# Optimization experiments

Measured on AMD Instinct MI355X. Metric: run time of the kernel, lower is better.

Reference implementation:

```python
import jax, jax.numpy as jnp
import numpy as np

N_HEAD = 16
N_KV_HEAD = 4
HEAD_DIM = 128  # n_embd // n_head = 2048 // 16


def _apply_rope(x, pos, T):
    # x: [B, H, T, D]; RoPE cache built exactly like the torch module:
    # cos/sin use repeat_interleave(2) on freqs, rotation uses half-split.
    D = x.shape[-1]
    half = D // 2
    inv_freq = 1.0 / jnp.power(10000.0, jnp.arange(0, D, 2, dtype=jnp.float32) / D)  # [half]
    t = jnp.arange(pos, pos + T, dtype=jnp.float32)                                  # [T]
    freqs = t[:, None] * inv_freq[None, :]                                           # [T, half]
    freqs = jnp.repeat(freqs, 2, axis=-1)                                            # [T, D]
    cos = jnp.cos(freqs)[None, None, :, :]
    sin = jnp.sin(freqs)[None, None, :, :]
    x1, x2 = x[..., :half], x[..., half:]
    rotated = jnp.concatenate([-x2, x1], axis=-1)
    return x * cos + rotated * sin


def setup_inputs() -> dict:
    key = jax.random.key(0)
    ks = jax.random.split(key, 5)
    B, T, E = 2, 2048, 2048
    KV = N_KV_HEAD * HEAD_DIM  # 512
    s = 0.02
    return {
        "x": jax.random.normal(ks[0], (B, T, E), dtype=jnp.float32),
        "Wq": jax.random.normal(ks[1], (E, E), dtype=jnp.float32) * s,
        "Wk": jax.random.normal(ks[2], (E, KV), dtype=jnp.float32) * s,
        "Wv": jax.random.normal(ks[3], (E, KV), dtype=jnp.float32) * s,
        "Wproj": jax.random.normal(ks[4], (E, E), dtype=jnp.float32) * s,
        "pos": 0,
    }


def reference(x, Wq, Wk, Wv, Wproj, pos):
    B, T, E = x.shape
    H, HKV, D = N_HEAD, N_KV_HEAD, HEAD_DIM
    G = H // HKV  # query heads per kv head

    q = (x @ Wq).reshape(B, T, H, D).transpose(0, 2, 1, 3)     # [B,H,T,D]
    k = (x @ Wk).reshape(B, T, HKV, D).transpose(0, 2, 1, 3)   # [B,HKV,T,D]
    v = (x @ Wv).reshape(B, T, HKV, D).transpose(0, 2, 1, 3)   # [B,HKV,T,D]

    q = _apply_rope(q, pos, T)
    k = _apply_rope(k, pos, T)

    # GQA: group query heads over shared kv heads
    qg = q.reshape(B, HKV, G, T, D)
    scale = 1.0 / jnp.sqrt(jnp.asarray(D, dtype=x.dtype))
    scores = jnp.einsum('bkgtd,bksd->bkgts', qg, k) * scale    # [B,HKV,G,T,T]

    causal = jnp.tril(jnp.ones((T, T), dtype=bool))
    scores = jnp.where(causal, scores, jnp.finfo(scores.dtype).min)
    attn = jax.nn.softmax(scores, axis=-1)

    out = jnp.einsum('bkgts,bksd->bkgtd', attn, v)             # [B,HKV,G,T,D]
    y = out.reshape(B, H, T, D).transpose(0, 2, 1, 3).reshape(B, T, E)
    return y @ Wproj
```

## Files before the change

### kernel.cpp

```cpp
#include <hip/hip_runtime.h>
#include <hip/hip_bf16.h>
#include <stdint.h>

typedef unsigned short u16;
typedef float f32x4 __attribute__((ext_vector_type(4)));
typedef __bf16 bf16x8 __attribute__((ext_vector_type(8)));
typedef unsigned short u16x8 __attribute__((ext_vector_type(8)));
typedef float f32x4v __attribute__((ext_vector_type(4)));

#define T_SEQ 2048

__device__ __forceinline__ u16 f2bf(float f) {
    unsigned int u = __float_as_uint(f);
    unsigned int r = (u + 0x7fffu + ((u >> 16) & 1u)) >> 16;
    return (u16)r;
}
__device__ __forceinline__ float bf2f(u16 b) {
    return __uint_as_float(((unsigned int)b) << 16);
}

__device__ __forceinline__ void gload_lds16(const void* g, void* l) {
    __builtin_amdgcn_global_load_lds(
        (__attribute__((address_space(1))) void*)(g),
        (__attribute__((address_space(3))) void*)(l), 16, 0, 0);
}

__global__ void cast_f32_bf16(const float* __restrict__ in, u16* __restrict__ out, int n8) {
    int i = blockIdx.x * blockDim.x + threadIdx.x;
    if (i >= n8) return;
    const f32x4v* p = (const f32x4v*)(in + (size_t)i * 8);
    f32x4v a = p[0], b = p[1];
    u16x8 v;
    v[0]=f2bf(a.x); v[1]=f2bf(a.y); v[2]=f2bf(a.z); v[3]=f2bf(a.w);
    v[4]=f2bf(b.x); v[5]=f2bf(b.y); v[6]=f2bf(b.z); v[7]=f2bf(b.w);
    *(u16x8*)(out + (size_t)i * 8) = v;
}

__global__ void transpose_cast(const float* __restrict__ W, u16* __restrict__ Wt, int N) {
    __shared__ alignas(16) float sW[64 * 68];
    const int t = threadIdx.x;
    const int k0 = blockIdx.x * 64, n0 = blockIdx.y * 64;
#pragma unroll
    for (int i = 0; i < 4; i++) {
        int kr = i * 16 + (t >> 4), nc = (t & 15) * 4;
        *(f32x4v*)&sW[kr * 68 + nc] = *(const f32x4v*)&W[(size_t)(k0 + kr) * N + n0 + nc];
    }
    __syncthreads();
#pragma unroll
    for (int i = 0; i < 2; i++) {
        int nr = i * 32 + (t >> 3), kc = (t & 7) * 8;
        u16x8 v;
#pragma unroll
        for (int j = 0; j < 8; j++) v[j] = f2bf(sW[(kc + j) * 68 + nr]);
        *(u16x8*)&Wt[(size_t)(n0 + nr) * 2048 + k0 + kc] = v;
    }
}

__device__ __forceinline__ void stage_rows(const u16* g, u16* lds, int R, int kcol0, int K, int t) {
    int row = R + (t >> 3);
    int u = t & 7;
    gload_lds16(g + (size_t)row * K + kcol0 + ((u ^ (row & 7)) * 8), lds + row * 64 + u * 8);
}
__device__ __forceinline__ void stage_half256(const u16* g, u16* lds, int half, int j, int kcol0, int K, int t) {
    int idx = j * 512 + t;
    int group = idx >> 8;
    int r32 = (idx >> 3) & 31;
    int row = group * 64 + half * 32 + r32;
    int u = idx & 7;
    gload_lds16(g + (size_t)row * K + kcol0 + ((u ^ (row & 7)) * 8), lds + row * 64 + u * 8);
}
__device__ __forceinline__ bf16x8 lds_ld(const u16* lds, int row, int kc, int hl) {
    return *(const bf16x8*)&lds[row * 64 + (((kc * 4 + hl) ^ (row & 7)) * 8)];
}

__global__ __launch_bounds__(512, 2) void gemm_qkv(const u16* __restrict__ A, const u16* __restrict__ Bt,
                                                   u16* __restrict__ C, int M, int N, int K) {
    __shared__ alignas(16) u16 ldsA[2][256 * 64];
    __shared__ alignas(16) u16 ldsB[2][192 * 64];
    const int t = threadIdx.x, wave = t >> 6, lane = t & 63;
    const int l15 = lane & 15, hl = lane >> 4;
    const int wr = wave >> 2, wc = wave & 3;

    const int f = blockIdx.x;
    const int swz = (f & 7) * 32 + (f >> 3);
    const int bx = swz & 15, by = swz >> 4;
    const int m0 = bx * 256, n0 = by * 192;

    const u16* gA = A + (size_t)m0 * K;
    const u16* gB = Bt + (size_t)n0 * K;

    f32x4 acc[8][3];
    f32x4 z = {0.f, 0.f, 0.f, 0.f};
#pragma unroll
    for (int m = 0; m < 8; m++)
#pragma unroll
        for (int n = 0; n < 3; n++) acc[m][n] = z;

    stage_rows(gA, ldsA[0], 0, 0, K, t);
    stage_rows(gA, ldsA[0], 128, 0, K, t);
    stage_rows(gB, ldsB[0], 0, 0, K, t);
    stage_rows(gB, ldsB[0], 64, 0, K, t);
    stage_rows(gB, ldsB[0], 128, 0, K, t);
    stage_rows(gA, ldsA[0], 64, 0, K, t);
    stage_rows(gA, ldsA[0], 192, 0, K, t);

    const int KT = K >> 6;
    for (int kt = 0; kt < KT; ++kt) {
        const int c = kt & 1;
        const int kn = (kt + 1 < KT) ? (kt + 1) * 64 : kt * 64;
        const u16* lAc = ldsA[c];
        const u16* lBc = ldsB[c];
        u16* lAn = ldsA[c ^ 1];
        u16* lBn = ldsB[c ^ 1];

        bf16x8 aF[4][2], bF[3][2];

        asm volatile("s_waitcnt vmcnt(2)" ::: "memory");
        __builtin_amdgcn_s_barrier();
#pragma unroll
        for (int mi = 0; mi < 4; mi++)
#pragma unroll
            for (int kc = 0; kc < 2; kc++)
                aF[mi][kc] = lds_ld(lAc, wr * 128 + mi * 16 + l15, kc, hl);
#pragma unroll
        for (int n = 0; n < 3; n++)
#pragma unroll
            for (int kc = 0; kc < 2; kc++)
                bF[n][kc] = lds_ld(lBc, wc * 48 + n * 16 + l15, kc, hl);
        stage_rows(gA, lAn, 0, kn, K, t);
        stage_rows(gA, lAn, 128, kn, K, t);
        stage_rows(gB, lBn, 0, kn, K, t);
        __builtin_amdgcn_s_setprio(1);
#pragma unroll
        for (int mi = 0; mi < 4; mi++)
#pragma unroll
            for (int n = 0; n < 3; n++)
#pragma unroll
                for (int kc = 0; kc < 2; kc++)
                    acc[mi][n] = __builtin_amdgcn_mfma_f32_16x16x32_bf16(aF[mi][kc], bF[n][kc], acc[mi][n], 0, 0, 0);
        __builtin_amdgcn_s_setprio(0);

        asm volatile("s_waitcnt vmcnt(3)" ::: "memory");
        __builtin_amdgcn_s_barrier();
#pragma unroll
        for (int mi = 0; mi < 4; mi++)
#pragma unroll
            for (int kc = 0; kc < 2; kc++)
                aF[mi][kc] = lds_ld(lAc, wr * 128 + 64 + mi * 16 + l15, kc, hl);
        stage_rows(gB, lBn, 64, kn, K, t);
        stage_rows(gB, lBn, 128, kn, K, t);
        stage_rows(gA, lAn, 64, kn, K, t);
        stage_rows(gA, lAn, 192, kn, K, t);
        __builtin_amdgcn_s_setprio(1);
#pragma unroll
        for (int mi = 0; mi < 4; mi++)
#pragma unroll
            for (int n = 0; n < 3; n++)
#pragma unroll
                for (int kc = 0; kc < 2; kc++)
                    acc[4 + mi][n] = __builtin_amdgcn_mfma_f32_16x16x32_bf16(aF[mi][kc], bF[n][kc], acc[4 + mi][n], 0, 0, 0);
        __builtin_amdgcn_s_setprio(0);
    }

#pragma unroll
    for (int m = 0; m < 8; m++)
#pragma unroll
        for (int n = 0; n < 3; n++)
#pragma unroll
            for (int r = 0; r < 4; r++) {
                int row = m0 + wr * 128 + m * 16 + hl * 4 + r;
                int col = n0 + wc * 48 + n * 16 + l15;
                C[(size_t)row * N + col] = f2bf(acc[m][n][r]);
            }
}

__global__ __launch_bounds__(512, 2) void gemm_proj(const u16* __restrict__ A, const u16* __restrict__ Bt,
                                                    float* __restrict__ C, int M, int N, int K) {
    __shared__ alignas(16) u16 ldsA[2][128 * 64];
    __shared__ alignas(16) u16 ldsB[2][256 * 64];
    const int t = threadIdx.x, wave = t >> 6, lane = t & 63;
    const int l15 = lane & 15, hl = lane >> 4;
    const int wr = wave >> 2, wc = wave & 3;

    const int f = blockIdx.x;
    const int swz = (f & 7) * 32 + (f >> 3);
    const int bx = swz & 31, by = swz >> 5;
    const int m0 = bx * 128, n0 = by * 256;

    const u16* gA = A + (size_t)m0 * K;
    const u16* gB = Bt + (size_t)n0 * K;

    f32x4 acc[4][4];
    f32x4 z = {0.f, 0.f, 0.f, 0.f};
#pragma unroll
    for (int m = 0; m < 4; m++)
#pragma unroll
        for (int n = 0; n < 4; n++) acc[m][n] = z;

    stage_rows(gA, ldsA[0], 0, 0, K, t);
    stage_rows(gA, ldsA[0], 64, 0, K, t);
    stage_half256(gB, ldsB[0], 0, 0, 0, K, t);
    stage_half256(gB, ldsB[0], 0, 1, 0, K, t);
    stage_half256(gB, ldsB[0], 1, 0, 0, K, t);
    stage_half256(gB, ldsB[0], 1, 1, 0, K, t);

    const int KT = K >> 6;
    for (int kt = 0; kt < KT; ++kt) {
        const int c = kt & 1;
        const int kn = (kt + 1 < KT) ? (kt + 1) * 64 : kt * 64;
        const u16* lAc = ldsA[c];
        const u16* lBc = ldsB[c];
        u16* lAn = ldsA[c ^ 1];
        u16* lBn = ldsB[c ^ 1];

        bf16x8 aF[4][2], bF[2][2];

        asm volatile("s_waitcnt vmcnt(2)" ::: "memory");
        __builtin_amdgcn_s_barrier();
#pragma unroll
        for (int mi = 0; mi < 4; mi++)
#pragma unroll
            for (int kc = 0; kc < 2; kc++)
                aF[mi][kc] = lds_ld(lAc, wr * 64 + mi * 16 + l15, kc, hl);
#pragma unroll
        for (int n = 0; n < 2; n++)
#pragma unroll
            for (int kc = 0; kc < 2; kc++)
                bF[n][kc] = lds_ld(lBc, wc * 64 + n * 16 + l15, kc, hl);
        stage_rows(gA, lAn, 0, kn, K, t);
        stage_rows(gA, lAn, 64, kn, K, t);
        stage_half256(gB, lBn, 0, 0, kn, K, t);
        stage_half256(gB, lBn, 0, 1, kn, K, t);
        __builtin_amdgcn_s_setprio(1);
#pragma unroll
        for (int mi = 0; mi < 4; mi++)
#pragma unroll
            for (int n = 0; n < 2; n++)
#pragma unroll
                for (int kc = 0; kc < 2; kc++)
                    acc[mi][n] = __builtin_amdgcn_mfma_f32_16x16x32_bf16(aF[mi][kc], bF[n][kc], acc[mi][n], 0, 0, 0);
        __builtin_amdgcn_s_setprio(0);

        asm volatile("s_waitcnt vmcnt(4)" ::: "memory");
        __builtin_amdgcn_s_barrier();
#pragma unroll
        for (int n = 0; n < 2; n++)
#pragma unroll
            for (int kc = 0; kc < 2; kc++)
                bF[n][kc] = lds_ld(lBc, wc * 64 + 32 + n * 16 + l15, kc, hl);
        stage_half256(gB, lBn, 1, 0, kn, K, t);
        stage_half256(gB, lBn, 1, 1, kn, K, t);
        __builtin_amdgcn_s_setprio(1);
#pragma unroll
        for (int mi = 0; mi < 4; mi++)
#pragma unroll
            for (int n = 0; n < 2; n++)
#pragma unroll
                for (int kc = 0; kc < 2; kc++)
                    acc[mi][2 + n] = __builtin_amdgcn_mfma_f32_16x16x32_bf16(aF[mi][kc], bF[n][kc], acc[mi][2 + n], 0, 0, 0);
        __builtin_amdgcn_s_setprio(0);
    }

#pragma unroll
    for (int m = 0; m < 4; m++)
#pragma unroll
        for (int n = 0; n < 4; n++)
#pragma unroll
            for (int r = 0; r < 4; r++) {
                int row = m0 + wr * 64 + m * 16 + hl * 4 + r;
                int col = n0 + wc * 64 + n * 16 + l15;
                C[(size_t)row * N + col] = acc[m][n][r];
            }
}

__global__ void rope_kernel(u16* __restrict__ qkv, const int* __restrict__ pos) {
    int tid = blockIdx.x * 256 + threadIdx.x;
    int j = tid & 63;
    int rest = tid >> 6;
    int slice = rest % 20;
    int row = rest / 20;
    if (row >= 2 * T_SEQ) return;
    float tpos = (float)((row % T_SEQ) + pos[0]);
    int base = (slice < 16) ? slice * 128 : 2048 + (slice - 16) * 128;
    u16* p = qkv + (size_t)row * 3072 + base;
    float x1 = bf2f(p[j]), x2 = bf2f(p[j + 64]);
    const float c0 = 0.20762050593045702f;
    int i = j >> 1;
    float fA = tpos * exp2f(-(float)i * c0);
    float fB = tpos * exp2f(-(float)(32 + i) * c0);
    float o1 = x1 * cosf(fA) - x2 * sinf(fA);
    float o2 = x2 * cosf(fB) + x1 * sinf(fB);
    p[j] = f2bf(o1);
    p[j + 64] = f2bf(o2);
}

__global__ void vtrans(const u16* __restrict__ qkv, u16* __restrict__ vt) {
    __shared__ alignas(16) u16 sT[64 * 72];
    const int t = threadIdx.x;
    const int t0 = blockIdx.x * 64;
    const int d0 = blockIdx.y * 64;
    const int kh = blockIdx.z & 3, b = blockIdx.z >> 2;
#pragma unroll
    for (int i = 0; i < 2; i++) {
        int tr = i * 32 + (t >> 3), dc = (t & 7) * 8;
        *(u16x8*)&sT[tr * 72 + dc] =
            *(const u16x8*)&qkv[(size_t)(b * T_SEQ + t0 + tr) * 3072 + 2560 + kh * 128 + d0 + dc];
    }
    __syncthreads();
#pragma unroll
    for (int i = 0; i < 2; i++) {
        int dr = i * 32 + (t >> 3), tc = (t & 7) * 8;
        u16x8 v;
#pragma unroll
        for (int j = 0; j < 8; j++) v[j] = sT[(tc + j) * 72 + dr];
        *(u16x8*)&vt[((size_t)(b * 4 + kh) * 128 + d0 + dr) * 2048 + t0 + tc] = v;
    }
}

__global__ __launch_bounds__(256, 2) void attn(const u16* __restrict__ qkv,
                                               const u16* __restrict__ vt,
                                               u16* __restrict__ out) {
    __shared__ alignas(16) u16 sK[2][8192];
    __shared__ alignas(16) u16 sV[8192];
    __shared__ alignas(16) u16 sP[4 * 32 * 72];
    const int t = threadIdx.x, wave = t >> 6, lane = t & 63;
    const int l15 = lane & 15, hl = lane >> 4;

    const int f = blockIdx.x;
    const int sel = f >> 8, u = f & 255;
    const int bkh = u & 7, b = bkh >> 2, kh = bkh & 3;
    const int h = kh * 4 + ((u >> 3) & 3);
    const int j = u >> 5;
    const int a = sel ? (15 - j) : j;
    const int q0 = a * 128;
    const int nt = 2 * a + 2;

    const float sc = 0.08838834764831845f;

    bf16x8 qf[2][4];
#pragma unroll
    for (int m = 0; m < 2; m++)
#pragma unroll
        for (int c = 0; c < 4; c++) {
            const u16* qp = qkv + (size_t)(b * T_SEQ + q0 + wave * 32 + m * 16 + l15) * 3072
                            + h * 128 + c * 32 + hl * 8;
            u16x8 raw = *(const u16x8*)qp;
            u16x8 sv_;
#pragma unroll
            for (int e = 0; e < 8; e++) sv_[e] = f2bf(bf2f(raw[e]) * sc);
            qf[m][c] = *(bf16x8*)&sv_;
        }

    u16x8 onesu;
#pragma unroll
    for (int e = 0; e < 8; e++) onesu[e] = 0x3F80;
    const bf16x8 onesf = *(bf16x8*)&onesu;

    float mrow[2][4];
    f32x4 o[2][8];
    f32x4 osum[2];
    f32x4 z = {0.f, 0.f, 0.f, 0.f};
#pragma unroll
    for (int m = 0; m < 2; m++) {
#pragma unroll
        for (int r = 0; r < 4; r++) mrow[m][r] = -1e30f;
        osum[m] = z;
#pragma unroll
        for (int n8 = 0; n8 < 8; n8++) o[m][n8] = z;
    }

    asm volatile("s_waitcnt vmcnt(0)" ::: "memory");

    const u16* kgbase = qkv + (size_t)(b * T_SEQ) * 3072 + 2048 + kh * 128;
    const u16* vgbase = vt + (size_t)(b * 4 + kh) * 128 * 2048;

#pragma unroll
    for (int p = 0; p < 4; p++) {
        int i = p * 256 + t;
        int row = i >> 4, c = i & 15;
        gload_lds16(kgbase + (size_t)row * 3072 + ((c ^ (row & 7)) * 8), (u16*)sK[0] + i * 8);
    }

    int cur = 0;
    for (int it = 0; it < nt; ++it) {
        const int kv0 = it * 64;
        const int kvn = (it + 1 < nt) ? kv0 + 64 : kv0;
#pragma unroll
        for (int p = 0; p < 4; p++) {
            int i = p * 256 + t;
            int row = i >> 3, c = i & 7;
            gload_lds16(vgbase + (size_t)row * 2048 + kv0 + ((c ^ (row & 7)) * 8), sV + i * 8);
        }
#pragma unroll
        for (int p = 0; p < 4; p++) {
            int i = p * 256 + t;
            int row = i >> 4, c = i & 15;
            gload_lds16(kgbase + (size_t)(kvn + row) * 3072 + ((c ^ (row & 7)) * 8),
                        (u16*)sK[cur ^ 1] + i * 8);
        }
        asm volatile("s_waitcnt vmcnt(8)" ::: "memory");
        __builtin_amdgcn_s_barrier();

        f32x4 sA[2][4];
#pragma unroll
        for (int m = 0; m < 2; m++)
#pragma unroll
            for (int n = 0; n < 4; n++) sA[m][n] = z;
#pragma unroll
        for (int n = 0; n < 4; n++)
#pragma unroll
            for (int c = 0; c < 4; c++) {
                int row = n * 16 + l15;
                bf16x8 kf = *(const bf16x8*)&sK[cur][row * 128 + (((c * 4 + hl) ^ (row & 7)) * 8)];
#pragma unroll
                for (int m = 0; m < 2; m++)
                    sA[m][n] = __builtin_amdgcn_mfma_f32_16x16x32_bf16(qf[m][c], kf, sA[m][n], 0, 0, 0);
            }

#pragma unroll
        for (int m = 0; m < 2; m++)
#pragma unroll
            for (int r = 0; r < 4; r++) {
                const int grow = q0 + wave * 32 + m * 16 + hl * 4 + r;
                float mv[4];
#pragma unroll
                for (int n = 0; n < 4; n++)
                    mv[n] = (kv0 + n * 16 + l15 <= grow) ? sA[m][n][r] : -1e30f;
                float pmax = fmaxf(fmaxf(mv[0], mv[1]), fmaxf(mv[2], mv[3]));
                if (__builtin_expect(__any(pmax > mrow[m][r] + 8.f), 0)) {
                    float mx = pmax;
#pragma unroll
                    for (int off = 1; off < 16; off <<= 1) mx = fmaxf(mx, __shfl_xor(mx, off));
                    float mnew = fmaxf(mrow[m][r], mx);
                    float alpha = __expf(mrow[m][r] - mnew);
                    mrow[m][r] = mnew;
#pragma unroll
                    for (int n8 = 0; n8 < 8; n8++) o[m][n8][r] *= alpha;
                    osum[m][r] *= alpha;
                }
#pragma unroll
                for (int n = 0; n < 4; n++)
                    sP[(wave * 32 + m * 16 + hl * 4 + r) * 72 + n * 16 + l15] =
                        f2bf(__expf(mv[n] - mrow[m][r]));
            }

        asm volatile("s_waitcnt vmcnt(4)" ::: "memory");
        __builtin_amdgcn_s_barrier();

        bf16x8 pa[2][2];
#pragma unroll
        for (int m = 0; m < 2; m++)
#pragma unroll
            for (int k2 = 0; k2 < 2; k2++)
                pa[m][k2] = *(const bf16x8*)&sP[(wave * 32 + m * 16 + l15) * 72 + k2 * 32 + hl * 8];
#pragma unroll
        for (int m = 0; m < 2; m++)
#pragma unroll
            for (int k2 = 0; k2 < 2; k2++)
                osum[m] = __builtin_amdgcn_mfma_f32_16x16x32_bf16(pa[m][k2], onesf, osum[m], 0, 0, 0);
#pragma unroll
        for (int n8 = 0; n8 < 8; n8++)
#pragma unroll
            for (int k2 = 0; k2 < 2; k2++) {
                int d = n8 * 16 + l15;
                bf16x8 vf = *(const bf16x8*)&sV[d * 64 + (((k2 * 4 + hl) ^ (d & 7)) * 8)];
#pragma unroll
                for (int m = 0; m < 2; m++)
                    o[m][n8] = __builtin_amdgcn_mfma_f32_16x16x32_bf16(pa[m][k2], vf, o[m][n8], 0, 0, 0);
            }
        __builtin_amdgcn_s_barrier();
        cur ^= 1;
    }

#pragma unroll
    for (int m = 0; m < 2; m++)
#pragma unroll
        for (int r = 0; r < 4; r++) {
            float inv = 1.f / osum[m][r];
            int orow = b * T_SEQ + q0 + wave * 32 + m * 16 + hl * 4 + r;
#pragma unroll
            for (int n8 = 0; n8 < 8; n8++)
                out[(size_t)orow * 2048 + h * 128 + n8 * 16 + l15] = f2bf(o[m][n8][r] * inv);
        }
}

extern "C" void kernel_launch(void* const* d_in, const int* in_sizes, int n_in,
                              void* d_out, int out_size, void* d_ws, size_t ws_size,
                              hipStream_t stream) {
    const float* x  = (const float*)d_in[0];
    const float* Wq = (const float*)d_in[1];
    const float* Wk = (const float*)d_in[2];
    const float* Wv = (const float*)d_in[3];
    const float* Wp = (const float*)d_in[4];
    const int*   pos = (const int*)d_in[5];

    char* ws = (char*)d_ws;
    u16* xbf   = (u16*)(ws);
    u16* WtQKV = (u16*)(ws + 16777216);
    u16* WtP   = (u16*)(ws + 29360128);
    u16* QKV   = (u16*)(ws + 37748736);
    u16* Vt    = (u16*)(ws + 62914560);
    u16* AO    = (u16*)(ws + 67108864);

    cast_f32_bf16<<<4096, 256, 0, stream>>>(x, xbf, 1048576);
    transpose_cast<<<dim3(32, 32), 256, 0, stream>>>(Wq, WtQKV, 2048);
    transpose_cast<<<dim3(32, 8), 256, 0, stream>>>(Wk, WtQKV + (size_t)2048 * 2048, 512);
    transpose_cast<<<dim3(32, 8), 256, 0, stream>>>(Wv, WtQKV + (size_t)2560 * 2048, 512);
    transpose_cast<<<dim3(32, 32), 256, 0, stream>>>(Wp, WtP, 2048);

    gemm_qkv<<<256, 512, 0, stream>>>(xbf, WtQKV, QKV, 4096, 3072, 2048);
    rope_kernel<<<20480, 256, 0, stream>>>(QKV, pos);
    vtrans<<<dim3(32, 2, 8), 256, 0, stream>>>(QKV, Vt);
    attn<<<512, 256, 0, stream>>>(QKV, Vt, AO);
    gemm_proj<<<256, 512, 0, stream>>>(AO, WtP, (float*)d_out, 4096, 2048, 2048);
}
```

Before: 212.1 us.

## Load V fragments directly into registers and drop V shared-memory staging

The attention kernel now reads V^T fragments straight from global memory into 16 registers per lane each iteration, instead of staging them through a swizzled LDS buffer. This frees the V LDS buffer and removes two of the three barriers per iteration. It also switches the bf16 conversions to hardware casts. The cost is higher register pressure under the launch_bounds(256,2) limit and uncoalesced global loads that each wave repeats. The barrier removal relies on sP being wave-private, and on the sK double buffer staying race-free with a single barrier per iteration.

New measurement: 257.3 us. 1.21x slower.

```diff
diff --git a/kernel.cpp b/kernel.cpp
--- a/kernel.cpp
+++ b/kernel.cpp
@@ -17,6 +17,10 @@
 }
 __device__ __forceinline__ float bf2f(u16 b) {
     return __uint_as_float(((unsigned int)b) << 16);
+}
+__device__ __forceinline__ u16 bfbits(float f) {
+    __bf16 h = (__bf16)f;
+    return __builtin_bit_cast(u16, h);
 }
 
 __device__ __forceinline__ void gload_lds16(const void* g, void* l) {
@@ -321,8 +325,7 @@
                                                const u16* __restrict__ vt,
                                                u16* __restrict__ out) {
     __shared__ alignas(16) u16 sK[2][8192];
-    __shared__ alignas(16) u16 sV[8192];
-    __shared__ alignas(16) u16 sP[4 * 32 * 72];
+    __shared__ alignas(16) __bf16 sP[4 * 32 * 72];
     const int t = threadIdx.x, wave = t >> 6, lane = t & 63;
     const int l15 = lane & 15, hl = lane >> 4;
 
@@ -372,7 +375,7 @@
     asm volatile("s_waitcnt vmcnt(0)" ::: "memory");
 
     const u16* kgbase = qkv + (size_t)(b * T_SEQ) * 3072 + 2048 + kh * 128;
-    const u16* vgbase = vt + (size_t)(b * 4 + kh) * 128 * 2048;
+    const u16* vbase = vt + ((size_t)(b * 4 + kh) * 128 + l15) * 2048 + hl * 8;
 
 #pragma unroll
     for (int p = 0; p < 4; p++) {
@@ -385,12 +388,17 @@
     for (int it = 0; it < nt; ++it) {
         const int kv0 = it * 64;
         const int kvn = (it + 1 < nt) ? kv0 + 64 : kv0;
-#pragma unroll
-        for (int p = 0; p < 4; p++) {
-            int i = p * 256 + t;
-            int row = i >> 3, c = i & 7;
-            gload_lds16(vgbase + (size_t)row * 2048 + kv0 + ((c ^ (row & 7)) * 8), sV + i * 8);
-        }
+
+        bf16x8 vf[16];
+#pragma unroll
+        for (int n8 = 0; n8 < 8; n8++)
+#pragma unroll
+            for (int k2 = 0; k2 < 2; k2++)
+                vf[n8 * 2 + k2] = *(const bf16x8*)(vbase + (size_t)(n8 * 16) * 2048 + kv0 + k2 * 32);
+
+        asm volatile("s_waitcnt vmcnt(16)" ::: "memory");
+        __builtin_amdgcn_s_barrier();
+
 #pragma unroll
         for (int p = 0; p < 4; p++) {
             int i = p * 256 + t;
@@ -398,8 +406,6 @@
             gload_lds16(kgbase + (size_t)(kvn + row) * 3072 + ((c ^ (row & 7)) * 8),
                         (u16*)sK[cur ^ 1] + i * 8);
         }
-        asm volatile("s_waitcnt vmcnt(8)" ::: "memory");
-        __builtin_amdgcn_s_barrier();
 
         f32x4 sA[2][4];
 #pragma unroll
@@ -441,11 +447,10 @@
 #pragma unroll
                 for (int n = 0; n < 4; n++)
                     sP[(wave * 32 + m * 16 + hl * 4 + r) * 72 + n * 16 + l15] =
-                        f2bf(__expf(mv[n] - mrow[m][r]));
+                        (__bf16)__expf(mv[n] - mrow[m][r]);
             }
 
         asm volatile("s_waitcnt vmcnt(4)" ::: "memory");
-        __builtin_amdgcn_s_barrier();
 
         bf16x8 pa[2][2];
 #pragma unroll
@@ -461,14 +466,10 @@
 #pragma unroll
         for (int n8 = 0; n8 < 8; n8++)
 #pragma unroll
-            for (int k2 = 0; k2 < 2; k2++) {
-                int d = n8 * 16 + l15;
-                bf16x8 vf = *(const bf16x8*)&sV[d * 64 + (((k2 * 4 + hl) ^ (d & 7)) * 8)];
+            for (int k2 = 0; k2 < 2; k2++)
 #pragma unroll
                 for (int m = 0; m < 2; m++)
-                    o[m][n8] = __builtin_amdgcn_mfma_f32_16x16x32_bf16(pa[m][k2], vf, o[m][n8], 0, 0, 0);
-            }
-        __builtin_amdgcn_s_barrier();
+                    o[m][n8] = __builtin_amdgcn_mfma_f32_16x16x32_bf16(pa[m][k2], vf[n8 * 2 + k2], o[m][n8], 0, 0, 0);
         cur ^= 1;
     }
 
@@ -480,7 +481,7 @@
             int orow = b * T_SEQ + q0 + wave * 32 + m * 16 + hl * 4 + r;
 #pragma unroll
             for (int n8 = 0; n8 < 8; n8++)
-                out[(size_t)orow * 2048 + h * 128 + n8 * 16 + l15] = f2bf(o[m][n8][r] * inv);
+                out[(size_t)orow * 2048 + h * 128 + n8 * 16 + l15] = bfbits(o[m][n8][r] * inv);
         }
 }
 
```
